# Kernel tuning notes

Measured on AMD Instinct MI355X. Metric: run time of the kernel, lower is better.

The kernel has to match this reference:

```python
import jax, jax.numpy as jnp
import numpy as np

B, S, H, R = 32, 512, 1024, 64


def _bernoulli(key, shape, p=0.05):
    return (jax.random.uniform(key, shape) < p).astype(jnp.float32)


def setup_inputs() -> dict:
    key = jax.random.key(0)
    ks = jax.random.split(key, 16)
    context = jax.random.normal(ks[0], (B, S, H), dtype=jnp.float32)
    masks = jnp.ones((B, S), dtype=jnp.float32)
    all_subject_heads = _bernoulli(ks[1], (B, S))
    all_subject_tails = _bernoulli(ks[2], (B, S))
    # one-hot subject head/tail positions (tail >= head)
    h_pos = jax.random.randint(ks[3], (B,), 0, S // 2)
    t_pos = h_pos + jax.random.randint(ks[4], (B,), 0, 8)
    subject_head = jax.nn.one_hot(h_pos, S, dtype=jnp.float32)
    subject_tail = jax.nn.one_hot(t_pos, S, dtype=jnp.float32)
    object_heads = _bernoulli(ks[5], (B, S, R))
    object_tails = _bernoulli(ks[6], (B, S, R))
    # learned parameters (PyTorch Linear: y = x @ W.T + b; store as [in, out])
    sc = 1.0 / np.sqrt(H)
    Ws_h = jax.random.uniform(ks[7], (H, 1), minval=-sc, maxval=sc)
    bs_h = jnp.zeros((1,), dtype=jnp.float32)
    Ws_t = jax.random.uniform(ks[8], (H, 1), minval=-sc, maxval=sc)
    bs_t = jnp.zeros((1,), dtype=jnp.float32)
    Wo_h = jax.random.uniform(ks[9], (H, R), minval=-sc, maxval=sc)
    bo_h = jnp.zeros((R,), dtype=jnp.float32)
    Wo_t = jax.random.uniform(ks[10], (H, R), minval=-sc, maxval=sc)
    bo_t = jnp.zeros((R,), dtype=jnp.float32)
    return dict(context=context, masks=masks,
                all_subject_heads=all_subject_heads, all_subject_tails=all_subject_tails,
                subject_head=subject_head, subject_tail=subject_tail,
                object_heads=object_heads, object_tails=object_tails,
                Ws_h=Ws_h, bs_h=bs_h, Ws_t=Ws_t, bs_t=bs_t,
                Wo_h=Wo_h, bo_h=bo_h, Wo_t=Wo_t, bo_t=bo_t)


def _bce_with_logits(logits, targets):
    # numerically stable, matches F.binary_cross_entropy_with_logits(reduction='none')
    return jnp.maximum(logits, 0.0) - logits * targets + jnp.log1p(jnp.exp(-jnp.abs(logits)))


def _masked_loss(gold, pred, mask):
    loss = _bce_with_logits(pred, gold)
    if loss.ndim != mask.ndim:
        mask = mask[..., None]
    return jnp.sum(loss * mask) / jnp.sum(mask)


def reference(context, masks, all_subject_heads, all_subject_tails,
              subject_head, subject_tail, object_heads, object_tails,
              Ws_h, bs_h, Ws_t, bs_t, Wo_h, bo_h, Wo_t, bo_t):
    # subject logits: [B,S]
    pred_subject_heads = (context @ Ws_h + bs_h)[..., 0]
    pred_subject_tails = (context @ Ws_t + bs_t)[..., 0]
    # subject pooling: one-hot [B,S] x context [B,S,H] -> [B,H]
    sub_h = jnp.einsum('bs,bsh->bh', subject_head, context)
    sub_t = jnp.einsum('bs,bsh->bh', subject_tail, context)
    subject = (sub_h + sub_t) * 0.5
    context_subject = context + subject[:, None, :]  # [B,S,H]
    pred_object_heads = context_subject @ Wo_h + bo_h  # [B,S,R]
    pred_object_tails = context_subject @ Wo_t + bo_t  # [B,S,R]
    loss = (_masked_loss(all_subject_heads, pred_subject_heads, masks)
            + _masked_loss(all_subject_tails, pred_subject_tails, masks)
            + _masked_loss(object_heads, pred_object_heads, masks)
            + _masked_loss(object_tails, pred_object_tails, masks))
    return loss
```

## Files before the change

### kernel.cpp

```cpp
#include <hip/hip_runtime.h>


#define B_  32
#define S_  512
#define H_  1024
#define R_  64
#define M_  (B_ * S_)
#define NPAD 160
#define NVALID 130
#define BK 128
#define BKP 136
#define MT 32
#define NCHUNK (H_ / BK)
#define TBLK 20

typedef __attribute__((ext_vector_type(4))) float  floatx4;
typedef __attribute__((ext_vector_type(8))) short  short8;
typedef __attribute__((ext_vector_type(4))) unsigned short u16x4;
typedef __attribute__((ext_vector_type(8))) unsigned short u16x8;

__device__ __forceinline__ unsigned short f2bf(float f) {
    unsigned int u = __float_as_uint(f);
    u = (u + 0x7FFFu + ((u >> 16) & 1u)) >> 16;
    return (unsigned short)u;
}

__device__ __forceinline__ u16x8 cvt8u(float4 a, float4 b) {
    u16x8 u;
    u[0] = f2bf(a.x); u[1] = f2bf(a.y); u[2] = f2bf(a.z); u[3] = f2bf(a.w);
    u[4] = f2bf(b.x); u[5] = f2bf(b.y); u[6] = f2bf(b.z); u[7] = f2bf(b.w);
    return u;
}

__global__ __launch_bounds__(256) void aux_kernel(
        const float* __restrict__ ctx, const float* __restrict__ head,
        const float* __restrict__ tail, const float* __restrict__ masks,
        const float* __restrict__ Wo_h, const float* __restrict__ Wo_t,
        const float* __restrict__ Ws_h, const float* __restrict__ Ws_t,
        const float* __restrict__ bo_h, const float* __restrict__ bo_t,
        const float* __restrict__ bs_h, const float* __restrict__ bs_t,
        unsigned short* __restrict__ WtG, float* __restrict__ rowBias,
        float* __restrict__ accum) {
    const int tid = threadIdx.x;
    __shared__ float tr[32][257];
    __shared__ float subj[H_];
    __shared__ float partS[4][256];
    __shared__ int cnt;
    __shared__ int   sidx[8];
    __shared__ float sw[8];

    if (blockIdx.x < TBLK) {
        const int kt = blockIdx.x / 5, nt = blockIdx.x % 5;
        const int k0 = kt * 256, n0 = nt * 32;
        if (n0 < 128) {
            const float* src = (n0 < 64) ? Wo_h : Wo_t;
            const int cb = n0 & 63;
            const int nn = tid & 31, kk = tid >> 5;
#pragma unroll
            for (int i = 0; i < 32; ++i) {
                const int k = k0 + i * 8 + kk;
                tr[nn][i * 8 + kk] = src[(size_t)k * R_ + cb + nn];
            }
            __syncthreads();
#pragma unroll
            for (int p = 0; p < 4; ++p) {
                const int chunk = p * 256 + tid;
                const int n = chunk >> 5;
                const int kc = (chunk & 31) * 8;
                u16x8 v;
#pragma unroll
                for (int j = 0; j < 8; ++j) v[j] = f2bf(tr[n][kc + j]);
                *(u16x8*)(WtG + (size_t)(n0 + n) * H_ + k0 + kc) = v;
            }
        } else {
#pragma unroll
            for (int p = 0; p < 4; ++p) {
                const int chunk = p * 256 + tid;
                const int n = 128 + (chunk >> 5);
                const int kc = (chunk & 31) * 8;
                u16x8 v;
#pragma unroll
                for (int j = 0; j < 8; ++j) {
                    float f = (n == 128) ? Ws_h[k0 + kc + j]
                            : (n == 129) ? Ws_t[k0 + kc + j] : 0.0f;
                    v[j] = f2bf(f);
                }
                *(u16x8*)(WtG + (size_t)n * H_ + k0 + kc) = v;
            }
        }
        return;
    }

    const int b = blockIdx.x - TBLK;
    if (tid == 0) cnt = 0;
    __syncthreads();
    float msk = 0.0f;
    for (int s = tid; s < S_; s += 256) {
        float w = 0.5f * (head[b * S_ + s] + tail[b * S_ + s]);
        if (w != 0.0f) {
            int i = atomicAdd(&cnt, 1);
            if (i < 8) { sidx[i] = s; sw[i] = w; }
        }
        msk += masks[b * S_ + s];
    }
    for (int o = 32; o > 0; o >>= 1) msk += __shfl_down(msk, o, 64);
    if ((tid & 63) == 0) atomicAdd(&accum[1], msk);
    __syncthreads();
    const int nnz = cnt < 8 ? cnt : 8;
    for (int h = tid; h < H_; h += 256) {
        float a = 0.0f;
        for (int i = 0; i < nnz; i++)
            a += sw[i] * ctx[((size_t)b * S_ + sidx[i]) * H_ + h];
        subj[h] = a;
    }
    __syncthreads();
    {
        const int cg = tid & 31;
        const int ks = tid >> 5;
        const int c4 = cg * 4;
        const float* W = (c4 < 64) ? Wo_h : Wo_t;
        const int cc = c4 & 63;
        const int kk0 = ks * 128;
        float ax = 0.f, ay = 0.f, az = 0.f, aw2 = 0.f;
#pragma unroll 4
        for (int k = kk0; k < kk0 + 128; ++k) {
            const float4 w = *(const float4*)(W + (size_t)k * R_ + cc);
            const float sv = subj[k];
            ax += sv * w.x; ay += sv * w.y; az += sv * w.z; aw2 += sv * w.w;
        }
        partS[0][tid] = ax; partS[1][tid] = ay;
        partS[2][tid] = az; partS[3][tid] = aw2;
    }
    __syncthreads();
    if (tid < NPAD) {
        float bias = tid < 64  ? bo_h[tid]
                   : tid < 128 ? bo_t[tid - 64]
                   : tid == 128 ? bs_h[0]
                   : tid == 129 ? bs_t[0] : 0.0f;
        float a2 = 0.0f;
        if (tid < 128) {
            const int g = tid >> 2, j = tid & 3;
#pragma unroll
            for (int s = 0; s < 8; ++s) a2 += partS[j][s * 32 + g];
        }
        rowBias[b * NPAD + tid] = bias + a2;
    }
}

__global__ __launch_bounds__(256, 2) void main_kernel(
        const float* __restrict__ ctx, const unsigned short* __restrict__ WtG,
        const float* __restrict__ rowBias, const float* __restrict__ masks,
        const float* __restrict__ ash, const float* __restrict__ ast,
        const float* __restrict__ oh, const float* __restrict__ ot,
        float* __restrict__ accum, float* __restrict__ out) {
    __shared__ __align__(16) unsigned short Asm[MT * BKP];
    __shared__ __align__(16) unsigned short Bsm[NPAD * BK];
    __shared__ float rbuf[4];

    const int tid  = threadIdx.x;
    const int gm0  = blockIdx.x * MT;
    const int b    = gm0 >> 9;
    const int wave = tid >> 6, lane = tid & 63;
    const int wm = wave & 1;
    const int wn = wave >> 1;
    const int lr = lane & 15, q = lane >> 4;

    const int ar = tid >> 3, as_ = (tid & 7) * 16;
    const float* aSrc = ctx + (size_t)(gm0 + ar) * H_ + as_;
    unsigned short* aDst = &Asm[ar * BKP + as_];

    const int br = tid >> 3, bs0 = (tid & 7) * 16;
    const unsigned short* bSrc = WtG + (size_t)br * H_ + bs0;
    const int bswz = (br & 7) << 4;
    char* bDstB = (char*)Bsm + br * 256;

    const int aOff = (wm * 16 + lr) * BKP + q * 8;
    int bOff[5];
#pragma unroll
    for (int tt = 0; tt < 5; ++tt) {
        const int row = wn * 80 + tt * 16 + lr;
        bOff[tt] = row * 256 + ((q * 16) ^ ((row & 7) << 4));
    }

    floatx4 acc[5];
#pragma unroll
    for (int tt = 0; tt < 5; ++tt) acc[tt] = (floatx4){0.f, 0.f, 0.f, 0.f};

    float4 aR[4];
    u16x8  bR[10];

#define LOADREGS(k0) do {                                                      \
        _Pragma("unroll")                                                      \
        for (int i = 0; i < 4; ++i)                                            \
            aR[i] = *(const float4*)(aSrc + (k0) + i * 4);                     \
        _Pragma("unroll")                                                      \
        for (int p = 0; p < 5; ++p) {                                          \
            bR[2*p]   = *(const u16x8*)(bSrc + (size_t)(p*32) * H_ + (k0));    \
            bR[2*p+1] = *(const u16x8*)(bSrc + (size_t)(p*32) * H_ + (k0) + 8);\
        }                                                                      \
    } while (0)

#define WRITE_LDS() do {                                                       \
        *(u16x8*)(aDst)     = cvt8u(aR[0], aR[1]);                             \
        *(u16x8*)(aDst + 8) = cvt8u(aR[2], aR[3]);                             \
        _Pragma("unroll")                                                      \
        for (int p = 0; p < 5; ++p) {                                          \
            *(u16x8*)(bDstB + p * 32 * 256 + ((bs0 * 2)      ^ bswz)) = bR[2*p];   \
            *(u16x8*)(bDstB + p * 32 * 256 + ((bs0 * 2 + 16) ^ bswz)) = bR[2*p+1]; \
        }                                                                      \
    } while (0)

    LOADREGS(0);
    for (int t = 0; t < NCHUNK; ++t) {
        __syncthreads();
        WRITE_LDS();
        if (t < NCHUNK - 1) LOADREGS((t + 1) * BK);
        __syncthreads();
#pragma unroll
        for (int kk = 0; kk < BK; kk += 32) {
            short8 afr = *(const short8*)&Asm[aOff + kk];
#pragma unroll
            for (int tt = 0; tt < 5; ++tt) {
                short8 bfr = *(const short8*)((const char*)Bsm + (bOff[tt] ^ (kk << 1)));
                acc[tt] = __builtin_amdgcn_mfma_f32_16x16x32_bf16(afr, bfr, acc[tt], 0, 0, 0);
            }
        }
    }
#undef LOADREGS
#undef WRITE_LDS

    float lsum = 0.0f;
#pragma unroll
    for (int tt = 0; tt < 5; ++tt) {
        const int col = wn * 80 + tt * 16 + lr;
        if (col < NVALID) {
            const float rb = rowBias[b * NPAD + col];
#pragma unroll
            for (int i = 0; i < 4; ++i) {
                const int row = gm0 + wm * 16 + q * 4 + i;
                const float l = acc[tt][i] + rb;
                float tgt;
                if (col < 64)        tgt = oh[(size_t)row * R_ + col];
                else if (col < 128)  tgt = ot[(size_t)row * R_ + (col - 64)];
                else if (col == 128) tgt = ash[row];
                else                 tgt = ast[row];
                const float mk = masks[row];
                const float bce = fmaxf(l, 0.0f) - l * tgt + log1pf(__expf(-fabsf(l)));
                lsum += bce * mk;
            }
        }
    }
    for (int o = 32; o > 0; o >>= 1) lsum += __shfl_down(lsum, o, 64);
    if (lane == 0) rbuf[wave] = lsum;
    __syncthreads();
    if (tid == 0) {
        atomicAdd(&accum[0], rbuf[0] + rbuf[1] + rbuf[2] + rbuf[3]);
        __threadfence();
        const unsigned int prev = atomicAdd((unsigned int*)(accum + 2), 1u);
        if (prev == gridDim.x - 1) {
            const float s = atomicAdd(&accum[0], 0.0f);
            const float m = atomicAdd(&accum[1], 0.0f);
            out[0] = s / m;
        }
    }
}

extern "C" void kernel_launch(void* const* d_in, const int* in_sizes, int n_in,
                              void* d_out, int out_size, void* d_ws, size_t ws_size,
                              hipStream_t stream) {
    const float* ctx   = (const float*)d_in[0];
    const float* masks = (const float*)d_in[1];
    const float* ash   = (const float*)d_in[2];
    const float* ast   = (const float*)d_in[3];
    const float* sh    = (const float*)d_in[4];
    const float* st    = (const float*)d_in[5];
    const float* oh    = (const float*)d_in[6];
    const float* ot    = (const float*)d_in[7];
    const float* Ws_h  = (const float*)d_in[8];
    const float* bs_h  = (const float*)d_in[9];
    const float* Ws_t  = (const float*)d_in[10];
    const float* bs_t  = (const float*)d_in[11];
    const float* Wo_h  = (const float*)d_in[12];
    const float* bo_h  = (const float*)d_in[13];
    const float* Wo_t  = (const float*)d_in[14];
    const float* bo_t  = (const float*)d_in[15];
    float* out = (float*)d_out;

    char* ws = (char*)d_ws;
    float* accum   = (float*)(ws + 0);
    float* rowBias = (float*)(ws + 256);
    unsigned short* WtG = (unsigned short*)(ws + 256 + 32 * NPAD * 4);

    hipMemsetAsync(accum, 0, 12, stream);
    aux_kernel<<<TBLK + B_, 256, 0, stream>>>(ctx, sh, st, masks, Wo_h, Wo_t,
                                              Ws_h, Ws_t, bo_h, bo_t, bs_h, bs_t,
                                              WtG, rowBias, accum);
    main_kernel<<<M_ / MT, 256, 0, stream>>>(ctx, WtG, rowBias, masks,
                                             ash, ast, oh, ot, accum, out);
}
```

Measured before the change: 165.4 us.

## Keep whole-K weight slice resident in LDS, stream context directly into MFMA

```diff
diff --git a/kernel.cpp b/kernel.cpp
--- a/kernel.cpp
+++ b/kernel.cpp
@@ -8,15 +8,14 @@
 #define M_  (B_ * S_)
 #define NPAD 160
 #define NVALID 130
-#define BK 128
-#define BKP 136
-#define MT 32
-#define NCHUNK (H_ / BK)
+#define MT 128
+#define CGC 80
 #define TBLK 20
+#define NTHR 512
+#define NKS (H_ / 32)
 
 typedef __attribute__((ext_vector_type(4))) float  floatx4;
 typedef __attribute__((ext_vector_type(8))) short  short8;
-typedef __attribute__((ext_vector_type(4))) unsigned short u16x4;
 typedef __attribute__((ext_vector_type(8))) unsigned short u16x8;
 
 __device__ __forceinline__ unsigned short f2bf(float f) {
@@ -25,11 +24,17 @@
     return (unsigned short)u;
 }
 
-__device__ __forceinline__ u16x8 cvt8u(float4 a, float4 b) {
-    u16x8 u;
-    u[0] = f2bf(a.x); u[1] = f2bf(a.y); u[2] = f2bf(a.z); u[3] = f2bf(a.w);
-    u[4] = f2bf(b.x); u[5] = f2bf(b.y); u[6] = f2bf(b.z); u[7] = f2bf(b.w);
-    return u;
+__device__ __forceinline__ short8 cvt8(float4 a, float4 b) {
+    union { unsigned short us[8]; short8 s8; } u;
+    u.us[0] = f2bf(a.x); u.us[1] = f2bf(a.y); u.us[2] = f2bf(a.z); u.us[3] = f2bf(a.w);
+    u.us[4] = f2bf(b.x); u.us[5] = f2bf(b.y); u.us[6] = f2bf(b.z); u.us[7] = f2bf(b.w);
+    return u.s8;
+}
+
+__device__ __forceinline__ void gload16(const void* g, void* l) {
+    __builtin_amdgcn_global_load_lds(
+        (const __attribute__((address_space(1))) unsigned int*)g,
+        (__attribute__((address_space(3))) unsigned int*)l, 16, 0, 0);
 }
 
 __global__ __launch_bounds__(256) void aux_kernel(
@@ -147,98 +152,71 @@
     }
 }
 
-__global__ __launch_bounds__(256, 2) void main_kernel(
+__global__ __launch_bounds__(NTHR) void main_kernel(
         const float* __restrict__ ctx, const unsigned short* __restrict__ WtG,
         const float* __restrict__ rowBias, const float* __restrict__ masks,
         const float* __restrict__ ash, const float* __restrict__ ast,
         const float* __restrict__ oh, const float* __restrict__ ot,
-        float* __restrict__ accum, float* __restrict__ out) {
-    __shared__ __align__(16) unsigned short Asm[MT * BKP];
-    __shared__ __align__(16) unsigned short Bsm[NPAD * BK];
-    __shared__ float rbuf[4];
+        float* __restrict__ accum, float* __restrict__ accumB,
+        float* __restrict__ out) {
+    __shared__ __align__(16) unsigned short Bsm[CGC * H_];
 
     const int tid  = threadIdx.x;
-    const int gm0  = blockIdx.x * MT;
+    const int bid  = blockIdx.x;
+    const int mb   = bid >> 1, cg = bid & 1;
+    const int gm0  = mb * MT;
     const int b    = gm0 >> 9;
     const int wave = tid >> 6, lane = tid & 63;
-    const int wm = wave & 1;
-    const int wn = wave >> 1;
     const int lr = lane & 15, q = lane >> 4;
-
-    const int ar = tid >> 3, as_ = (tid & 7) * 16;
-    const float* aSrc = ctx + (size_t)(gm0 + ar) * H_ + as_;
-    unsigned short* aDst = &Asm[ar * BKP + as_];
-
-    const int br = tid >> 3, bs0 = (tid & 7) * 16;
-    const unsigned short* bSrc = WtG + (size_t)br * H_ + bs0;
-    const int bswz = (br & 7) << 4;
-    char* bDstB = (char*)Bsm + br * 256;
-
-    const int aOff = (wm * 16 + lr) * BKP + q * 8;
-    int bOff[5];
-#pragma unroll
-    for (int tt = 0; tt < 5; ++tt) {
-        const int row = wn * 80 + tt * 16 + lr;
-        bOff[tt] = row * 256 + ((q * 16) ^ ((row & 7) << 4));
-    }
+    const int col0 = cg * CGC;
+
+#pragma unroll
+    for (int p = 0; p < (CGC * H_ * 2 / 16) / NTHR; ++p) {
+        const int i = p * NTHR + tid;
+        const int row = i >> 7;
+        const int bytecol = (i & 127) << 4;
+        const int srcb = bytecol ^ ((row & 7) << 4);
+        gload16((const char*)(WtG + (size_t)(col0 + row) * H_) + srcb,
+                (char*)Bsm + i * 16);
+    }
+    __syncthreads();
+
+    const int arow = gm0 + wave * 16 + lr;
+    const float* aP = ctx + (size_t)arow * H_ + q * 8;
+    const int swz = (lr & 7) << 4;
+    const int oe = (q << 4) ^ swz;
+    const int oo = (64 | (q << 4)) ^ swz;
+    int rb5[5];
+#pragma unroll
+    for (int t = 0; t < 5; ++t) rb5[t] = (t * 16 + lr) * 2048;
 
     floatx4 acc[5];
 #pragma unroll
-    for (int tt = 0; tt < 5; ++tt) acc[tt] = (floatx4){0.f, 0.f, 0.f, 0.f};
-
-    float4 aR[4];
-    u16x8  bR[10];
-
-#define LOADREGS(k0) do {                                                      \
-        _Pragma("unroll")                                                      \
-        for (int i = 0; i < 4; ++i)                                            \
-            aR[i] = *(const float4*)(aSrc + (k0) + i * 4);                     \
-        _Pragma("unroll")                                                      \
-        for (int p = 0; p < 5; ++p) {                                          \
-            bR[2*p]   = *(const u16x8*)(bSrc + (size_t)(p*32) * H_ + (k0));    \
-            bR[2*p+1] = *(const u16x8*)(bSrc + (size_t)(p*32) * H_ + (k0) + 8);\
-        }                                                                      \
-    } while (0)
-
-#define WRITE_LDS() do {                                                       \
-        *(u16x8*)(aDst)     = cvt8u(aR[0], aR[1]);                             \
-        *(u16x8*)(aDst + 8) = cvt8u(aR[2], aR[3]);                             \
-        _Pragma("unroll")                                                      \
-        for (int p = 0; p < 5; ++p) {                                          \
-            *(u16x8*)(bDstB + p * 32 * 256 + ((bs0 * 2)      ^ bswz)) = bR[2*p];   \
-            *(u16x8*)(bDstB + p * 32 * 256 + ((bs0 * 2 + 16) ^ bswz)) = bR[2*p+1]; \
-        }                                                                      \
-    } while (0)
-
-    LOADREGS(0);
-    for (int t = 0; t < NCHUNK; ++t) {
-        __syncthreads();
-        WRITE_LDS();
-        if (t < NCHUNK - 1) LOADREGS((t + 1) * BK);
-        __syncthreads();
-#pragma unroll
-        for (int kk = 0; kk < BK; kk += 32) {
-            short8 afr = *(const short8*)&Asm[aOff + kk];
-#pragma unroll
-            for (int tt = 0; tt < 5; ++tt) {
-                short8 bfr = *(const short8*)((const char*)Bsm + (bOff[tt] ^ (kk << 1)));
-                acc[tt] = __builtin_amdgcn_mfma_f32_16x16x32_bf16(afr, bfr, acc[tt], 0, 0, 0);
-            }
-        }
-    }
-#undef LOADREGS
-#undef WRITE_LDS
+    for (int t = 0; t < 5; ++t) acc[t] = (floatx4){0.f, 0.f, 0.f, 0.f};
+
+#pragma unroll
+    for (int kk = 0; kk < NKS; ++kk) {
+        const float4 f0 = *(const float4*)(aP + kk * 32);
+        const float4 f1 = *(const float4*)(aP + kk * 32 + 4);
+        const short8 afr = cvt8(f0, f1);
+        const int kb = (kk >> 1) * 128 + ((kk & 1) ? oo : oe);
+#pragma unroll
+        for (int t = 0; t < 5; ++t) {
+            const short8 bfr = *(const short8*)((const char*)Bsm + rb5[t] + kb);
+            acc[t] = __builtin_amdgcn_mfma_f32_16x16x32_bf16(afr, bfr, acc[t], 0, 0, 0);
+        }
+    }
 
     float lsum = 0.0f;
 #pragma unroll
-    for (int tt = 0; tt < 5; ++tt) {
-        const int col = wn * 80 + tt * 16 + lr;
+    for (int t = 0; t < 5; ++t) {
+        const int col = col0 + t * 16 + lr;
         if (col < NVALID) {
-            const float rb = rowBias[b * NPAD + col];
+            const float rbv = rowBias[b * NPAD + col];
 #pragma unroll
             for (int i = 0; i < 4; ++i) {
-                const int row = gm0 + wm * 16 + q * 4 + i;
-                const float l = acc[tt][i] + rb;
+                const int row = gm0 + wave * 16 + q * 4 + i;
+                const float l = acc[t][i] + rbv;
                 float tgt;
                 if (col < 64)        tgt = oh[(size_t)row * R_ + col];
                 else if (col < 128)  tgt = ot[(size_t)row * R_ + (col - 64)];
@@ -251,10 +229,11 @@
         }
     }
     for (int o = 32; o > 0; o >>= 1) lsum += __shfl_down(lsum, o, 64);
-    if (lane == 0) rbuf[wave] = lsum;
+    if (lane == 0) atomicAdd(&accumB[bid], lsum);
     __syncthreads();
     if (tid == 0) {
-        atomicAdd(&accum[0], rbuf[0] + rbuf[1] + rbuf[2] + rbuf[3]);
+        const float s0 = atomicAdd(&accumB[bid], 0.0f);
+        atomicAdd(&accum[0], s0);
         __threadfence();
         const unsigned int prev = atomicAdd((unsigned int*)(accum + 2), 1u);
         if (prev == gridDim.x - 1) {
@@ -288,13 +267,15 @@
 
     char* ws = (char*)d_ws;
     float* accum   = (float*)(ws + 0);
-    float* rowBias = (float*)(ws + 256);
-    unsigned short* WtG = (unsigned short*)(ws + 256 + 32 * NPAD * 4);
-
-    hipMemsetAsync(accum, 0, 12, stream);
+    float* accumB  = (float*)(ws + 256);
+    float* rowBias = (float*)(ws + 2048);
+    unsigned short* WtG = (unsigned short*)(ws + 2048 + 32 * NPAD * 4);
+
+    hipMemsetAsync(ws, 0, 1280, stream);
     aux_kernel<<<TBLK + B_, 256, 0, stream>>>(ctx, sh, st, masks, Wo_h, Wo_t,
                                               Ws_h, Ws_t, bo_h, bo_t, bs_h, bs_t,
                                               WtG, rowBias, accum);
-    main_kernel<<<M_ / MT, 256, 0, stream>>>(ctx, WtG, rowBias, masks,
-                                             ash, ast, oh, ot, accum, out);
-}
+    main_kernel<<<(M_ / MT) * 2, NTHR, 0, stream>>>(ctx, WtG, rowBias, masks,
+                                                    ash, ast, oh, ot,
+                                                    accum, accumB, out);
+}
```

Result: slower. 177.3 us (+7.2%).

## Double row tile to 64 so each block reuses weight tile across two MFMA rows

Applied to the files above, without the earlier changes.

```diff
diff --git a/kernel.cpp b/kernel.cpp
--- a/kernel.cpp
+++ b/kernel.cpp
@@ -10,9 +10,10 @@
 #define NVALID 130
 #define BK 128
 #define BKP 136
-#define MT 32
+#define MT 64
 #define NCHUNK (H_ / BK)
 #define TBLK 20
+#define NTHR 256
 
 typedef __attribute__((ext_vector_type(4))) float  floatx4;
 typedef __attribute__((ext_vector_type(8))) short  short8;
@@ -147,7 +148,7 @@
     }
 }
 
-__global__ __launch_bounds__(256, 2) void main_kernel(
+__global__ __launch_bounds__(NTHR, 2) void main_kernel(
         const float* __restrict__ ctx, const unsigned short* __restrict__ WtG,
         const float* __restrict__ rowBias, const float* __restrict__ masks,
         const float* __restrict__ ash, const float* __restrict__ ast,
@@ -165,16 +166,23 @@
     const int wn = wave >> 1;
     const int lr = lane & 15, q = lane >> 4;
 
-    const int ar = tid >> 3, as_ = (tid & 7) * 16;
-    const float* aSrc = ctx + (size_t)(gm0 + ar) * H_ + as_;
-    unsigned short* aDst = &Asm[ar * BKP + as_];
-
-    const int br = tid >> 3, bs0 = (tid & 7) * 16;
-    const unsigned short* bSrc = WtG + (size_t)br * H_ + bs0;
-    const int bswz = (br & 7) << 4;
-    char* bDstB = (char*)Bsm + br * 256;
-
-    const int aOff = (wm * 16 + lr) * BKP + q * 8;
+    const int ar0 = tid >> 3,        as0 = (tid & 7) * 16;
+    const int ar1 = (tid + 256) >> 3;
+    const float* aSrc0 = ctx + (size_t)(gm0 + ar0) * H_ + as0;
+    const float* aSrc1 = ctx + (size_t)(gm0 + ar1) * H_ + as0;
+    unsigned short* aDst0 = &Asm[ar0 * BKP + as0];
+    unsigned short* aDst1 = &Asm[ar1 * BKP + as0];
+
+    const int br0 = tid >> 3, br1 = (tid + 256) >> 3;
+    const int bs0 = (tid & 7) * 16;
+    const unsigned short* bSrc0 = WtG + (size_t)br0 * H_ + bs0;
+    const unsigned short* bSrc1 = WtG + (size_t)br1 * H_ + bs0;
+    const int bswz0 = (br0 & 7) << 4, bswz1 = (br1 & 7) << 4;
+    char* bDst0 = (char*)Bsm + br0 * 256;
+    char* bDst1 = (char*)Bsm + br1 * 256;
+
+    const int aOffA = (wm * 32 + lr) * BKP + q * 8;
+    const int aOffB = aOffA + 16 * BKP;
     int bOff[5];
 #pragma unroll
     for (int tt = 0; tt < 5; ++tt) {
@@ -182,32 +190,49 @@
         bOff[tt] = row * 256 + ((q * 16) ^ ((row & 7) << 4));
     }
 
-    floatx4 acc[5];
-#pragma unroll
-    for (int tt = 0; tt < 5; ++tt) acc[tt] = (floatx4){0.f, 0.f, 0.f, 0.f};
-
-    float4 aR[4];
+    floatx4 acc[5], acc2[5];
+#pragma unroll
+    for (int tt = 0; tt < 5; ++tt) {
+        acc[tt]  = (floatx4){0.f, 0.f, 0.f, 0.f};
+        acc2[tt] = (floatx4){0.f, 0.f, 0.f, 0.f};
+    }
+
+    float4 aR[8];
     u16x8  bR[10];
 
 #define LOADREGS(k0) do {                                                      \
         _Pragma("unroll")                                                      \
-        for (int i = 0; i < 4; ++i)                                            \
-            aR[i] = *(const float4*)(aSrc + (k0) + i * 4);                     \
-        _Pragma("unroll")                                                      \
-        for (int p = 0; p < 5; ++p) {                                          \
-            bR[2*p]   = *(const u16x8*)(bSrc + (size_t)(p*32) * H_ + (k0));    \
-            bR[2*p+1] = *(const u16x8*)(bSrc + (size_t)(p*32) * H_ + (k0) + 8);\
+        for (int i = 0; i < 4; ++i) {                                          \
+            aR[i]     = *(const float4*)(aSrc0 + (k0) + i * 4);                \
+            aR[4 + i] = *(const float4*)(aSrc1 + (k0) + i * 4);                \
         }                                                                      \
+        bR[0] = *(const u16x8*)(bSrc0 + (k0));                                 \
+        bR[1] = *(const u16x8*)(bSrc0 + (k0) + 8);                             \
+        bR[2] = *(const u16x8*)(bSrc0 + (size_t)64 * H_ + (k0));               \
+        bR[3] = *(const u16x8*)(bSrc0 + (size_t)64 * H_ + (k0) + 8);           \
+        bR[4] = *(const u16x8*)(bSrc0 + (size_t)128 * H_ + (k0));              \
+        bR[5] = *(const u16x8*)(bSrc0 + (size_t)128 * H_ + (k0) + 8);          \
+        bR[6] = *(const u16x8*)(bSrc1 + (k0));                                 \
+        bR[7] = *(const u16x8*)(bSrc1 + (k0) + 8);                             \
+        bR[8] = *(const u16x8*)(bSrc1 + (size_t)64 * H_ + (k0));               \
+        bR[9] = *(const u16x8*)(bSrc1 + (size_t)64 * H_ + (k0) + 8);           \
     } while (0)
 
 #define WRITE_LDS() do {                                                       \
-        *(u16x8*)(aDst)     = cvt8u(aR[0], aR[1]);                             \
-        *(u16x8*)(aDst + 8) = cvt8u(aR[2], aR[3]);                             \
-        _Pragma("unroll")                                                      \
-        for (int p = 0; p < 5; ++p) {                                          \
-            *(u16x8*)(bDstB + p * 32 * 256 + ((bs0 * 2)      ^ bswz)) = bR[2*p];   \
-            *(u16x8*)(bDstB + p * 32 * 256 + ((bs0 * 2 + 16) ^ bswz)) = bR[2*p+1]; \
-        }                                                                      \
+        *(u16x8*)(aDst0)     = cvt8u(aR[0], aR[1]);                            \
+        *(u16x8*)(aDst0 + 8) = cvt8u(aR[2], aR[3]);                            \
+        *(u16x8*)(aDst1)     = cvt8u(aR[4], aR[5]);                            \
+        *(u16x8*)(aDst1 + 8) = cvt8u(aR[6], aR[7]);                            \
+        *(u16x8*)(bDst0 + ((bs0 * 2)      ^ bswz0)) = bR[0];                   \
+        *(u16x8*)(bDst0 + ((bs0 * 2 + 16) ^ bswz0)) = bR[1];                   \
+        *(u16x8*)(bDst0 + 64 * 256 + ((bs0 * 2)      ^ bswz0)) = bR[2];        \
+        *(u16x8*)(bDst0 + 64 * 256 + ((bs0 * 2 + 16) ^ bswz0)) = bR[3];        \
+        *(u16x8*)(bDst0 + 128 * 256 + ((bs0 * 2)      ^ bswz0)) = bR[4];       \
+        *(u16x8*)(bDst0 + 128 * 256 + ((bs0 * 2 + 16) ^ bswz0)) = bR[5];       \
+        *(u16x8*)(bDst1 + ((bs0 * 2)      ^ bswz1)) = bR[6];                   \
+        *(u16x8*)(bDst1 + ((bs0 * 2 + 16) ^ bswz1)) = bR[7];                   \
+        *(u16x8*)(bDst1 + 64 * 256 + ((bs0 * 2)      ^ bswz1)) = bR[8];        \
+        *(u16x8*)(bDst1 + 64 * 256 + ((bs0 * 2 + 16) ^ bswz1)) = bR[9];        \
     } while (0)
 
     LOADREGS(0);
@@ -218,11 +243,13 @@
         __syncthreads();
 #pragma unroll
         for (int kk = 0; kk < BK; kk += 32) {
-            short8 afr = *(const short8*)&Asm[aOff + kk];
+            short8 afr0 = *(const short8*)&Asm[aOffA + kk];
+            short8 afr1 = *(const short8*)&Asm[aOffB + kk];
 #pragma unroll
             for (int tt = 0; tt < 5; ++tt) {
                 short8 bfr = *(const short8*)((const char*)Bsm + (bOff[tt] ^ (kk << 1)));
-                acc[tt] = __builtin_amdgcn_mfma_f32_16x16x32_bf16(afr, bfr, acc[tt], 0, 0, 0);
+                acc[tt]  = __builtin_amdgcn_mfma_f32_16x16x32_bf16(afr0, bfr, acc[tt],  0, 0, 0);
+                acc2[tt] = __builtin_amdgcn_mfma_f32_16x16x32_bf16(afr1, bfr, acc2[tt], 0, 0, 0);
             }
         }
     }
@@ -237,16 +264,19 @@
             const float rb = rowBias[b * NPAD + col];
 #pragma unroll
             for (int i = 0; i < 4; ++i) {
-                const int row = gm0 + wm * 16 + q * 4 + i;
-                const float l = acc[tt][i] + rb;
-                float tgt;
-                if (col < 64)        tgt = oh[(size_t)row * R_ + col];
-                else if (col < 128)  tgt = ot[(size_t)row * R_ + (col - 64)];
-                else if (col == 128) tgt = ash[row];
-                else                 tgt = ast[row];
-                const float mk = masks[row];
-                const float bce = fmaxf(l, 0.0f) - l * tgt + log1pf(__expf(-fabsf(l)));
-                lsum += bce * mk;
+#pragma unroll
+                for (int h = 0; h < 2; ++h) {
+                    const int row = gm0 + wm * 32 + h * 16 + q * 4 + i;
+                    const float l = (h ? acc2[tt][i] : acc[tt][i]) + rb;
+                    float tgt;
+                    if (col < 64)        tgt = oh[(size_t)row * R_ + col];
+                    else if (col < 128)  tgt = ot[(size_t)row * R_ + (col - 64)];
+                    else if (col == 128) tgt = ash[row];
+                    else                 tgt = ast[row];
+                    const float mk = masks[row];
+                    const float bce = fmaxf(l, 0.0f) - l * tgt + log1pf(__expf(-fabsf(l)));
+                    lsum += bce * mk;
+                }
             }
         }
     }
@@ -295,6 +325,6 @@
     aux_kernel<<<TBLK + B_, 256, 0, stream>>>(ctx, sh, st, masks, Wo_h, Wo_t,
                                               Ws_h, Ws_t, bo_h, bo_t, bs_h, bs_t,
                                               WtG, rowBias, accum);
-    main_kernel<<<M_ / MT, 256, 0, stream>>>(ctx, WtG, rowBias, masks,
-                                             ash, ast, oh, ot, accum, out);
-}
+    main_kernel<<<M_ / MT, NTHR, 0, stream>>>(ctx, WtG, rowBias, masks,
+                                              ash, ast, oh, ot, accum, out);
+}
```

Result: faster. 161.6 us, median of 2 (-2.3%).
